# Kernel optimization log

Hardware: AMD Instinct MI355X
Metric: run time of the kernel (lower is better)

## Reference

```python
import jax, jax.numpy as jnp
import numpy as np

D_MODEL = 1024
NUM_HEADS = 16
HEAD_DIM = D_MODEL // NUM_HEADS


def setup_inputs() -> dict:
    key = jax.random.key(0)
    ks = jax.random.split(key, 9)
    s = 0.02
    return {
        "x": jax.random.normal(ks[0], (4, 2048, D_MODEL), dtype=jnp.float32),
        "Wq": jax.random.normal(ks[1], (D_MODEL, D_MODEL), dtype=jnp.float32) * s,
        "bq": jnp.zeros((D_MODEL,), dtype=jnp.float32),
        "Wk": jax.random.normal(ks[2], (D_MODEL, D_MODEL), dtype=jnp.float32) * s,
        "bk": jnp.zeros((D_MODEL,), dtype=jnp.float32),
        "Wv": jax.random.normal(ks[3], (D_MODEL, D_MODEL), dtype=jnp.float32) * s,
        "bv": jnp.zeros((D_MODEL,), dtype=jnp.float32),
        "Wo": jax.random.normal(ks[4], (D_MODEL, D_MODEL), dtype=jnp.float32) * s,
        "bo": jnp.zeros((D_MODEL,), dtype=jnp.float32),
    }


def reference(x, Wq, bq, Wk, bk, Wv, bv, Wo, bo):
    B, S, D = x.shape
    H, Hd = NUM_HEADS, HEAD_DIM

    def split_heads(t):  # [B,S,D] -> [B,H,S,Hd]
        return t.reshape(B, S, H, Hd).transpose(0, 2, 1, 3)

    q = split_heads(x @ Wq + bq)
    k = split_heads(x @ Wk + bk)
    v = split_heads(x @ Wv + bv)

    scale = 1.0 / jnp.sqrt(jnp.float32(Hd))
    scores = jnp.einsum("bhqd,bhkd->bhqk", q, k) * scale  # [B,H,S,S]
    attn = jax.nn.softmax(scores, axis=-1)
    # dropout(p=0.1) is identity in eval mode
    ctx = jnp.einsum("bhqk,bhkd->bhqd", attn, v)
    ctx = ctx.transpose(0, 2, 1, 3).reshape(B, S, D)
    return ctx @ Wo + bo
```

## Files before the change

kernel.cpp:

```cpp
#include <hip/hip_runtime.h>
#include <hip/hip_bf16.h>

typedef __bf16 bf16;
typedef bf16 bf16x8 __attribute__((ext_vector_type(8)));
typedef bf16 bf16x4v __attribute__((ext_vector_type(4)));
typedef bf16 bf16x2v __attribute__((ext_vector_type(2)));
typedef float f32x4 __attribute__((ext_vector_type(4)));
typedef float f32x16 __attribute__((ext_vector_type(16)));
typedef unsigned int uint;
typedef uint uint4v __attribute__((ext_vector_type(4)));

#define D_MODEL 1024
#define SEQ     2048
#define BATCH   4
#define NHEAD   16
#define HDIM    64
#define MTOK    8192
#define RSZ     ((size_t)MTOK * D_MODEL)
#define QSCALE  0.18033688011112042f

#define GLD16(src, dst)                                                        \
  __builtin_amdgcn_global_load_lds(                                            \
      (const __attribute__((address_space(1))) void*)(src),                    \
      (__attribute__((address_space(3))) void*)(dst), 16, 0, 0)

#define PSWAP(a, b) asm("v_permlane32_swap_b32 %0, %1" : "+v"(a), "+v"(b))

__device__ __forceinline__ uint pk2(float lo, float hi) {
  bf16x2v h;
  h[0] = (bf16)lo;
  h[1] = (bf16)hi;
  return __builtin_bit_cast(uint, h);
}

__global__ __launch_bounds__(256) void cvt_x_kernel(const float* __restrict__ x,
                                                    bf16* __restrict__ xb) {
  int i = blockIdx.x * 256 + threadIdx.x;
  f32x4 v = ((const f32x4*)x)[i];
  bf16x4v o;
#pragma unroll
  for (int c = 0; c < 4; ++c) o[c] = (bf16)v[c];
  ((bf16x4v*)xb)[i] = o;
}

__global__ __launch_bounds__(256) void wtrans_kernel(
    const float* __restrict__ Wq, const float* __restrict__ Wk,
    const float* __restrict__ Wv, const float* __restrict__ Wo,
    bf16* __restrict__ wt, bf16* __restrict__ wot) {
  __shared__ float t[32][33];
  int z = blockIdx.z;
  const float* W = (z == 0) ? Wq : (z == 1) ? Wk : (z == 2) ? Wv : Wo;
  bf16* dst = (z < 3) ? (wt + (size_t)z * D_MODEL * D_MODEL) : wot;
  int tx = threadIdx.x, ty = threadIdx.y;
  int bx = blockIdx.x * 32, by = blockIdx.y * 32;
#pragma unroll
  for (int j = 0; j < 4; ++j)
    t[ty + j * 8][tx] = W[(size_t)(by + ty + j * 8) * D_MODEL + bx + tx];
  __syncthreads();
#pragma unroll
  for (int j = 0; j < 4; ++j)
    dst[(size_t)(bx + ty + j * 8) * D_MODEL + by + tx] = (bf16)t[tx][ty + j * 8];
}

template <int MODE>
__global__ __launch_bounds__(256) void gemm_bt(
    const bf16* __restrict__ A, const bf16* __restrict__ Bt,
    const float* __restrict__ bias0, const float* __restrict__ bias1,
    const float* __restrict__ bias2, void* __restrict__ outp) {
  __shared__ bf16 As[128 * 32];
  __shared__ bf16 Bs[128 * 32];
  const int tid = threadIdx.x;
  const int wave = tid >> 6, lane = tid & 63;
  const int rowBase = blockIdx.y * 128;
  const int colBase = blockIdx.x * 128;
  const int wR = (wave >> 1) * 64;
  const int wC = (wave & 1) * 64;

  const int r0 = tid >> 2, c0 = tid & 3;
  const int cp0 = c0 ^ ((r0 >> 1) & 3);
  const int r1 = 64 + r0;
  const int cp1 = c0 ^ ((r1 >> 1) & 3);
  const bf16* srcA0 = A + (size_t)(rowBase + r0) * 1024 + cp0 * 8;
  const bf16* srcA1 = A + (size_t)(rowBase + r1) * 1024 + cp1 * 8;
  const bf16* srcB0 = Bt + (size_t)(colBase + r0) * 1024 + cp0 * 8;
  const bf16* srcB1 = Bt + (size_t)(colBase + r1) * 1024 + cp1 * 8;
  char* AsB = (char*)As;
  char* BsB = (char*)Bs;
  char* ldsA0 = AsB + wave * 1024;
  char* ldsA1 = AsB + 4096 + wave * 1024;
  char* ldsB0 = BsB + wave * 1024;
  char* ldsB1 = BsB + 4096 + wave * 1024;

  int aoff[4], boff[4];
#pragma unroll
  for (int i = 0; i < 4; ++i) {
    int ra = wR + i * 16 + (lane & 15);
    aoff[i] = ra * 64 + (((lane >> 4) ^ ((ra >> 1) & 3)) * 16);
    int rb = wC + i * 16 + (lane & 15);
    boff[i] = rb * 64 + (((lane >> 4) ^ ((rb >> 1) & 3)) * 16);
  }

  f32x4 acc[4][4] = {};
  for (int k0 = 0; k0 < 1024; k0 += 32) {
    GLD16(srcA0 + k0, ldsA0);
    GLD16(srcA1 + k0, ldsA1);
    GLD16(srcB0 + k0, ldsB0);
    GLD16(srcB1 + k0, ldsB1);
    __syncthreads();
    bf16x8 af[4], bf_[4];
#pragma unroll
    for (int i = 0; i < 4; ++i) af[i] = *(const bf16x8*)(AsB + aoff[i]);
#pragma unroll
    for (int i = 0; i < 4; ++i) bf_[i] = *(const bf16x8*)(BsB + boff[i]);
#pragma unroll
    for (int mi = 0; mi < 4; ++mi)
#pragma unroll
      for (int ni = 0; ni < 4; ++ni)
        acc[mi][ni] =
            __builtin_amdgcn_mfma_f32_16x16x32_bf16(af[mi], bf_[ni], acc[mi][ni], 0, 0, 0);
    __syncthreads();
  }

  const int rl = (lane >> 4) * 4;
  const int cl = lane & 15;
  if (MODE == 0) {
    bf16* qkvb = (bf16*)outp;
#pragma unroll
    for (int mi = 0; mi < 4; ++mi) {
      int rbase = rowBase + wR + mi * 16 + rl;
#pragma unroll
      for (int ni = 0; ni < 4; ++ni) {
        int col = colBase + wC + ni * 16 + cl;
        int mat = col >> 10, nn = col & 1023;
        int hh = nn >> 6, dd = nn & 63;
        if (mat == 2) {
          float bvv = bias2[nn];
          bf16x4v p4;
#pragma unroll
          for (int r = 0; r < 4; ++r) p4[r] = (bf16)(acc[mi][ni][r] + bvv);
          int bb = rbase >> 11, ss = rbase & 2047;
          *(bf16x4v*)(qkvb + 2 * RSZ +
                      ((size_t)(bb * NHEAD + hh) * HDIM + dd) * SEQ + ss) = p4;
        } else {
          const float* bp = (mat == 0) ? bias0 : bias1;
          float scl = (mat == 0) ? QSCALE : 1.0f;
          float bvv = bp[nn];
          bf16* dst = qkvb + (size_t)mat * RSZ;
#pragma unroll
          for (int r = 0; r < 4; ++r) {
            int m = rbase + r;
            int bb = m >> 11, ss = m & 2047;
            dst[((size_t)(bb * NHEAD + hh) * SEQ + ss) * HDIM + dd] =
                (bf16)((acc[mi][ni][r] + bvv) * scl);
          }
        }
      }
    }
  } else {
    float* dst = (float*)outp;
#pragma unroll
    for (int mi = 0; mi < 4; ++mi) {
      int rbase = rowBase + wR + mi * 16 + rl;
#pragma unroll
      for (int ni = 0; ni < 4; ++ni) {
        int col = colBase + wC + ni * 16 + cl;
        float bvv = bias0[col];
#pragma unroll
        for (int r = 0; r < 4; ++r)
          dst[(size_t)(rbase + r) * 1024 + col] = acc[mi][ni][r] + bvv;
      }
    }
  }
}

__global__ __launch_bounds__(256, 3) void attn_kernel(const bf16* __restrict__ qkv,
                                                      bf16* __restrict__ ctx) {
  __shared__ __align__(16) char smem[32768];
  char* Kbuf = smem;
  char* Vbuf = smem + 16384;

  const int tid = threadIdx.x;
  const int wave = tid >> 6, lane = tid & 63;
  const int l31 = lane & 31, l5 = lane >> 5;
  const int qt = blockIdx.x, hh = blockIdx.y, bb = blockIdx.z;
  const int bh = bb * NHEAD + hh;
  const bf16* Qp = qkv + (size_t)bh * SEQ * HDIM;
  const bf16* Kp = qkv + RSZ + (size_t)bh * SEQ * HDIM;
  const bf16* Vtp = qkv + 2 * RSZ + (size_t)bh * HDIM * SEQ;

  const int qrow = qt * 128 + wave * 32 + l31;
  bf16x8 qf[4];
#pragma unroll
  for (int kc = 0; kc < 4; ++kc)
    qf[kc] = *(const bf16x8*)(Qp + (size_t)qrow * 64 + kc * 16 + l5 * 8);

  const int sr = tid >> 3;
  const int sz = (tid & 7) ^ (sr & 7);
  const bf16* srcK0 = Kp + sr * 64 + sz * 8;
  const bf16* srcK1 = Kp + (sr + 32) * 64 + sz * 8;
  const bf16* srcV0 = Vtp + (size_t)sr * SEQ + sz * 8;
  const bf16* srcV1 = Vtp + (size_t)(sr + 32) * SEQ + sz * 8;

#define STAGE(sel, t)                                                     \
  do {                                                                    \
    GLD16(srcK0 + (t) * 4096, Kbuf + (sel) * 8192 + wave * 1024);         \
    GLD16(srcK1 + (t) * 4096, Kbuf + (sel) * 8192 + 4096 + wave * 1024);  \
    GLD16(srcV0 + (t) * 64, Vbuf + (sel) * 8192 + wave * 1024);           \
    GLD16(srcV1 + (t) * 64, Vbuf + (sel) * 8192 + 4096 + wave * 1024);    \
  } while (0)

  f32x16 o[2];
#pragma unroll
  for (int nd = 0; nd < 2; ++nd)
#pragma unroll
    for (int r = 0; r < 16; ++r) o[nd][r] = 0.f;
  float m_run = -1e30f, l_run = 0.f;

  STAGE(0, 0);
  __syncthreads();

  for (int kt = 0; kt < 32; ++kt) {
    const int cur = kt & 1;
    if (kt < 31) STAGE(cur ^ 1, kt + 1);

    const char* Kc = Kbuf + cur * 8192;
    const char* Vc = Vbuf + cur * 8192;

    f32x16 s[2];
#pragma unroll
    for (int nb = 0; nb < 2; ++nb)
#pragma unroll
      for (int r = 0; r < 16; ++r) s[nb][r] = 0.f;
#pragma unroll
    for (int nb = 0; nb < 2; ++nb)
#pragma unroll
      for (int kc = 0; kc < 4; ++kc) {
        int row = nb * 32 + l31;
        int off = row * 128 + (((2 * kc + l5) ^ (row & 7)) * 16);
        bf16x8 kf = *(const bf16x8*)(Kc + off);
        s[nb] = __builtin_amdgcn_mfma_f32_32x32x16_bf16(kf, qf[kc], s[nb], 0, 0, 0);
      }

    float t8[8];
#pragma unroll
    for (int r = 0; r < 8; ++r)
      t8[r] = fmaxf(fmaxf(s[0][r], s[0][r + 8]), fmaxf(s[1][r], s[1][r + 8]));
#pragma unroll
    for (int r = 0; r < 4; ++r) t8[r] = fmaxf(t8[r], t8[r + 4]);
    float pmax = fmaxf(fmaxf(t8[0], t8[1]), fmaxf(t8[2], t8[3]));
    pmax = fmaxf(pmax, __shfl_xor(pmax, 32, 64));

    if (!__all(pmax - m_run <= 8.0f)) {
      float mnew = fmaxf(m_run, pmax);
      float al = __builtin_amdgcn_exp2f(m_run - mnew);
      m_run = mnew;
      l_run *= al;
#pragma unroll
      for (int nd = 0; nd < 2; ++nd)
#pragma unroll
        for (int r = 0; r < 16; ++r) o[nd][r] *= al;
    }
#pragma unroll
    for (int nb = 0; nb < 2; ++nb)
#pragma unroll
      for (int r = 0; r < 16; ++r)
        s[nb][r] = __builtin_amdgcn_exp2f(s[nb][r] - m_run);

    f32x16 tv = s[0] + s[1];
    float q8[8];
#pragma unroll
    for (int r = 0; r < 8; ++r) q8[r] = tv[r] + tv[r + 8];
#pragma unroll
    for (int r = 0; r < 4; ++r) q8[r] += q8[r + 4];
    float rs = (q8[0] + q8[1]) + (q8[2] + q8[3]);
    rs += __shfl_xor(rs, 32, 64);
    l_run += rs;

    bf16x8 pf[4];
#pragma unroll
    for (int cc = 0; cc < 4; ++cc) {
      const int nb = cc >> 1, b0 = (cc & 1) * 8;
      uint w0 = pk2(s[nb][b0 + 0], s[nb][b0 + 1]);
      uint w1 = pk2(s[nb][b0 + 2], s[nb][b0 + 3]);
      uint w2 = pk2(s[nb][b0 + 4], s[nb][b0 + 5]);
      uint w3 = pk2(s[nb][b0 + 6], s[nb][b0 + 7]);
      PSWAP(w0, w2);
      PSWAP(w1, w3);
      uint4v u = {w0, w1, w2, w3};
      pf[cc] = __builtin_bit_cast(bf16x8, u);
    }

#pragma unroll
    for (int nd = 0; nd < 2; ++nd)
#pragma unroll
      for (int cc = 0; cc < 4; ++cc) {
        int row = nd * 32 + l31;
        int off = row * 128 + (((2 * cc + l5) ^ (row & 7)) * 16);
        bf16x8 vf = *(const bf16x8*)(Vc + off);
        o[nd] = __builtin_amdgcn_mfma_f32_32x32x16_bf16(vf, pf[cc], o[nd], 0, 0, 0);
      }
    __syncthreads();
  }

  const float inv = 1.0f / l_run;
  bf16* crow = ctx + (size_t)(bb * SEQ + qrow) * D_MODEL + hh * HDIM;
#pragma unroll
  for (int nd = 0; nd < 2; ++nd)
#pragma unroll
    for (int a = 0; a < 4; ++a) {
      bf16x4v p4;
#pragma unroll
      for (int b = 0; b < 4; ++b) p4[b] = (bf16)(o[nd][4 * a + b] * inv);
      *(bf16x4v*)(crow + nd * 32 + a * 8 + l5 * 4) = p4;
    }
#undef STAGE
}

extern "C" void kernel_launch(void* const* d_in, const int* in_sizes, int n_in,
                              void* d_out, int out_size, void* d_ws, size_t ws_size,
                              hipStream_t stream) {
  const float* x  = (const float*)d_in[0];
  const float* Wq = (const float*)d_in[1];
  const float* bq = (const float*)d_in[2];
  const float* Wk = (const float*)d_in[3];
  const float* bk = (const float*)d_in[4];
  const float* Wv = (const float*)d_in[5];
  const float* bv = (const float*)d_in[6];
  const float* Wo = (const float*)d_in[7];
  const float* bo = (const float*)d_in[8];

  char* ws = (char*)d_ws;
  bf16* xb   = (bf16*)(ws);
  bf16* wt   = (bf16*)(ws + (size_t)16 * 1024 * 1024);
  bf16* wot  = (bf16*)(ws + (size_t)22 * 1024 * 1024);
  bf16* qkvb = (bf16*)(ws + (size_t)24 * 1024 * 1024);
  bf16* ctxb = (bf16*)(ws + (size_t)72 * 1024 * 1024);

  cvt_x_kernel<<<8192, 256, 0, stream>>>(x, xb);
  wtrans_kernel<<<dim3(32, 32, 4), dim3(32, 8), 0, stream>>>(Wq, Wk, Wv, Wo, wt, wot);
  gemm_bt<0><<<dim3(24, 64), 256, 0, stream>>>(xb, wt, bq, bk, bv, (void*)qkvb);
  attn_kernel<<<dim3(16, 16, 4), 256, 0, stream>>>(qkvb, ctxb);
  gemm_bt<1><<<dim3(8, 64), 256, 0, stream>>>(ctxb, wot, bo, bo, bo, d_out);
}
```

Before: 295.8 us.

## Double-buffer GEMM LDS loads, swizzle block order for XCDs, add MFMA priority hints

The GEMM now double-buffers its A/B tiles in LDS, prefetching the next K slice while computing the current one. It replaces __syncthreads with explicit vmcnt waits plus raw barriers in both the GEMM and the attention kernel. Both kernels switch to 1D grids with a block-index swizzle that groups neighbouring tiles per XCD for better L2 locality, and the attention kernel raises wave priority around its MFMA sections. This doubles GEMM LDS use (lower occupancy risk) and depends on the hand-counted vmcnt values being correct.

```diff
diff --git a/kernel.cpp b/kernel.cpp
--- a/kernel.cpp
+++ b/kernel.cpp
@@ -23,6 +23,9 @@
   __builtin_amdgcn_global_load_lds(                                            \
       (const __attribute__((address_space(1))) void*)(src),                    \
       (__attribute__((address_space(3))) void*)(dst), 16, 0, 0)
+
+#define WAITVM(N) asm volatile("s_waitcnt vmcnt(" #N ")" ::: "memory")
+#define BAR() __builtin_amdgcn_s_barrier()
 
 #define PSWAP(a, b) asm("v_permlane32_swap_b32 %0, %1" : "+v"(a), "+v"(b))
 
@@ -67,12 +70,15 @@
     const bf16* __restrict__ A, const bf16* __restrict__ Bt,
     const float* __restrict__ bias0, const float* __restrict__ bias1,
     const float* __restrict__ bias2, void* __restrict__ outp) {
-  __shared__ bf16 As[128 * 32];
-  __shared__ bf16 Bs[128 * 32];
+  __shared__ bf16 As[2][128 * 32];
+  __shared__ bf16 Bs[2][128 * 32];
   const int tid = threadIdx.x;
   const int wave = tid >> 6, lane = tid & 63;
-  const int rowBase = blockIdx.y * 128;
-  const int colBase = blockIdx.x * 128;
+
+  const int nwg = gridDim.x;
+  const int swz = (blockIdx.x & 7) * (nwg >> 3) + (blockIdx.x >> 3);
+  const int rowBase = (swz & 63) * 128;
+  const int colBase = (swz >> 6) * 128;
   const int wR = (wave >> 1) * 64;
   const int wC = (wave & 1) * 64;
 
@@ -84,12 +90,14 @@
   const bf16* srcA1 = A + (size_t)(rowBase + r1) * 1024 + cp1 * 8;
   const bf16* srcB0 = Bt + (size_t)(colBase + r0) * 1024 + cp0 * 8;
   const bf16* srcB1 = Bt + (size_t)(colBase + r1) * 1024 + cp1 * 8;
-  char* AsB = (char*)As;
-  char* BsB = (char*)Bs;
-  char* ldsA0 = AsB + wave * 1024;
-  char* ldsA1 = AsB + 4096 + wave * 1024;
-  char* ldsB0 = BsB + wave * 1024;
-  char* ldsB1 = BsB + 4096 + wave * 1024;
+
+#define GSTAGE(sel, k0)                                                  \
+  do {                                                                   \
+    GLD16(srcA0 + (k0), (char*)As[sel] + wave * 1024);                   \
+    GLD16(srcA1 + (k0), (char*)As[sel] + 4096 + wave * 1024);            \
+    GLD16(srcB0 + (k0), (char*)Bs[sel] + wave * 1024);                   \
+    GLD16(srcB1 + (k0), (char*)Bs[sel] + 4096 + wave * 1024);            \
+  } while (0)
 
   int aoff[4], boff[4];
 #pragma unroll
@@ -101,12 +109,18 @@
   }
 
   f32x4 acc[4][4] = {};
-  for (int k0 = 0; k0 < 1024; k0 += 32) {
-    GLD16(srcA0 + k0, ldsA0);
-    GLD16(srcA1 + k0, ldsA1);
-    GLD16(srcB0 + k0, ldsB0);
-    GLD16(srcB1 + k0, ldsB1);
-    __syncthreads();
+  GSTAGE(0, 0);
+  for (int t = 0; t < 32; ++t) {
+    const int cur = t & 1;
+    if (t < 31) {
+      GSTAGE(cur ^ 1, (t + 1) * 32);
+      WAITVM(4);
+    } else {
+      WAITVM(0);
+    }
+    BAR();
+    const char* AsB = (const char*)As[cur];
+    const char* BsB = (const char*)Bs[cur];
     bf16x8 af[4], bf_[4];
 #pragma unroll
     for (int i = 0; i < 4; ++i) af[i] = *(const bf16x8*)(AsB + aoff[i]);
@@ -118,8 +132,9 @@
       for (int ni = 0; ni < 4; ++ni)
         acc[mi][ni] =
             __builtin_amdgcn_mfma_f32_16x16x32_bf16(af[mi], bf_[ni], acc[mi][ni], 0, 0, 0);
-    __syncthreads();
+    BAR();
   }
+#undef GSTAGE
 
   const int rl = (lane >> 4) * 4;
   const int cl = lane & 15;
@@ -182,7 +197,8 @@
   const int tid = threadIdx.x;
   const int wave = tid >> 6, lane = tid & 63;
   const int l31 = lane & 31, l5 = lane >> 5;
-  const int qt = blockIdx.x, hh = blockIdx.y, bb = blockIdx.z;
+  const int swz = (blockIdx.x & 7) * 128 + (blockIdx.x >> 3);
+  const int qt = swz & 15, hh = (swz >> 4) & 15, bb = swz >> 8;
   const int bh = bb * NHEAD + hh;
   const bf16* Qp = qkv + (size_t)bh * SEQ * HDIM;
   const bf16* Kp = qkv + RSZ + (size_t)bh * SEQ * HDIM;
@@ -217,11 +233,16 @@
   float m_run = -1e30f, l_run = 0.f;
 
   STAGE(0, 0);
-  __syncthreads();
 
   for (int kt = 0; kt < 32; ++kt) {
     const int cur = kt & 1;
-    if (kt < 31) STAGE(cur ^ 1, kt + 1);
+    if (kt < 31) {
+      STAGE(cur ^ 1, kt + 1);
+      WAITVM(4);
+    } else {
+      WAITVM(0);
+    }
+    BAR();
 
     const char* Kc = Kbuf + cur * 8192;
     const char* Vc = Vbuf + cur * 8192;
@@ -231,6 +252,7 @@
     for (int nb = 0; nb < 2; ++nb)
 #pragma unroll
       for (int r = 0; r < 16; ++r) s[nb][r] = 0.f;
+    __builtin_amdgcn_s_setprio(1);
 #pragma unroll
     for (int nb = 0; nb < 2; ++nb)
 #pragma unroll
@@ -240,6 +262,7 @@
         bf16x8 kf = *(const bf16x8*)(Kc + off);
         s[nb] = __builtin_amdgcn_mfma_f32_32x32x16_bf16(kf, qf[kc], s[nb], 0, 0, 0);
       }
+    __builtin_amdgcn_s_setprio(0);
 
     float t8[8];
 #pragma unroll
@@ -290,6 +313,7 @@
       pf[cc] = __builtin_bit_cast(bf16x8, u);
     }
 
+    __builtin_amdgcn_s_setprio(1);
 #pragma unroll
     for (int nd = 0; nd < 2; ++nd)
 #pragma unroll
@@ -299,7 +323,8 @@
         bf16x8 vf = *(const bf16x8*)(Vc + off);
         o[nd] = __builtin_amdgcn_mfma_f32_32x32x16_bf16(vf, pf[cc], o[nd], 0, 0, 0);
       }
-    __syncthreads();
+    __builtin_amdgcn_s_setprio(0);
+    BAR();
   }
 
   const float inv = 1.0f / l_run;
@@ -338,7 +363,7 @@
 
   cvt_x_kernel<<<8192, 256, 0, stream>>>(x, xb);
   wtrans_kernel<<<dim3(32, 32, 4), dim3(32, 8), 0, stream>>>(Wq, Wk, Wv, Wo, wt, wot);
-  gemm_bt<0><<<dim3(24, 64), 256, 0, stream>>>(xb, wt, bq, bk, bv, (void*)qkvb);
-  attn_kernel<<<dim3(16, 16, 4), 256, 0, stream>>>(qkvb, ctxb);
-  gemm_bt<1><<<dim3(8, 64), 256, 0, stream>>>(ctxb, wot, bo, bo, bo, d_out);
-}
+  gemm_bt<0><<<1536, 256, 0, stream>>>(xb, wt, bq, bk, bv, (void*)qkvb);
+  attn_kernel<<<1024, 256, 0, stream>>>(qkvb, ctxb);
+  gemm_bt<1><<<512, 256, 0, stream>>>(ctxb, wot, bo, bo, bo, d_out);
+}
```

Result: slower. 319.2 us (+7.9%).

## Move V transpose to separate kernel, swizzle attention grid, relax LDS barrier waits

Applied to the files above, without the earlier changes.

The QKV GEMM now writes V in the same row-major head layout as Q and K, and a new kernel transposes V into a separate buffer that reuses the x workspace. The attention kernel remaps its flat grid so consecutive blocks spread across heads and batches. It replaces the end-of-iteration syncthreads with explicit vmcnt waits plus a barrier so the prefetch of the next tile overlaps compute. It also raises wave priority around the MFMA sections. The goal is to drop the scattered transposed stores from the GEMM epilogue and hide load latency, at the cost of an extra kernel launch and another full pass over V.

```diff
diff --git a/kernel.cpp b/kernel.cpp
--- a/kernel.cpp
+++ b/kernel.cpp
@@ -23,6 +23,9 @@
   __builtin_amdgcn_global_load_lds(                                            \
       (const __attribute__((address_space(1))) void*)(src),                    \
       (__attribute__((address_space(3))) void*)(dst), 16, 0, 0)
+
+#define WAITVM(N) asm volatile("s_waitcnt vmcnt(" #N ")" ::: "memory")
+#define BAR() __builtin_amdgcn_s_barrier()
 
 #define PSWAP(a, b) asm("v_permlane32_swap_b32 %0, %1" : "+v"(a), "+v"(b))
 
@@ -60,6 +63,28 @@
 #pragma unroll
   for (int j = 0; j < 4; ++j)
     dst[(size_t)(bx + ty + j * 8) * D_MODEL + by + tx] = (bf16)t[tx][ty + j * 8];
+}
+
+__global__ __launch_bounds__(256) void vtrans_kernel(const bf16* __restrict__ V,
+                                                     bf16* __restrict__ Vt) {
+  __shared__ bf16 Ls[128][72];
+  const int st = blockIdx.x, bh = blockIdx.y;
+  const bf16* src = V + ((size_t)bh * SEQ + st * 128) * HDIM;
+  bf16* dst = Vt + (size_t)bh * HDIM * SEQ + st * 128;
+  const int t = threadIdx.x;
+  const int r = t >> 3, d0 = (t & 7) * 8;
+#pragma unroll
+  for (int j = 0; j < 4; ++j)
+    *(bf16x8*)&Ls[r + j * 32][d0] = *(const bf16x8*)(src + (size_t)(r + j * 32) * HDIM + d0);
+  __syncthreads();
+  const int d = t & 63, sc = (t >> 6) * 32;
+#pragma unroll
+  for (int c = 0; c < 4; ++c) {
+    bf16x8 v;
+#pragma unroll
+    for (int i = 0; i < 8; ++i) v[i] = Ls[sc + c * 8 + i][d];
+    *(bf16x8*)(dst + (size_t)d * SEQ + sc + c * 8) = v;
+  }
 }
 
 template <int MODE>
@@ -133,26 +158,16 @@
         int col = colBase + wC + ni * 16 + cl;
         int mat = col >> 10, nn = col & 1023;
         int hh = nn >> 6, dd = nn & 63;
-        if (mat == 2) {
-          float bvv = bias2[nn];
-          bf16x4v p4;
-#pragma unroll
-          for (int r = 0; r < 4; ++r) p4[r] = (bf16)(acc[mi][ni][r] + bvv);
-          int bb = rbase >> 11, ss = rbase & 2047;
-          *(bf16x4v*)(qkvb + 2 * RSZ +
-                      ((size_t)(bb * NHEAD + hh) * HDIM + dd) * SEQ + ss) = p4;
-        } else {
-          const float* bp = (mat == 0) ? bias0 : bias1;
-          float scl = (mat == 0) ? QSCALE : 1.0f;
-          float bvv = bp[nn];
-          bf16* dst = qkvb + (size_t)mat * RSZ;
-#pragma unroll
-          for (int r = 0; r < 4; ++r) {
-            int m = rbase + r;
-            int bb = m >> 11, ss = m & 2047;
-            dst[((size_t)(bb * NHEAD + hh) * SEQ + ss) * HDIM + dd] =
-                (bf16)((acc[mi][ni][r] + bvv) * scl);
-          }
+        const float* bp = (mat == 0) ? bias0 : (mat == 1) ? bias1 : bias2;
+        float scl = (mat == 0) ? QSCALE : 1.0f;
+        float bvv = bp[nn];
+        bf16* dst = qkvb + (size_t)mat * RSZ;
+#pragma unroll
+        for (int r = 0; r < 4; ++r) {
+          int m = rbase + r;
+          int bb = m >> 11, ss = m & 2047;
+          dst[((size_t)(bb * NHEAD + hh) * SEQ + ss) * HDIM + dd] =
+              (bf16)((acc[mi][ni][r] + bvv) * scl);
         }
       }
     }
@@ -174,6 +189,7 @@
 }
 
 __global__ __launch_bounds__(256, 3) void attn_kernel(const bf16* __restrict__ qkv,
+                                                      const bf16* __restrict__ vt,
                                                       bf16* __restrict__ ctx) {
   __shared__ __align__(16) char smem[32768];
   char* Kbuf = smem;
@@ -182,11 +198,12 @@
   const int tid = threadIdx.x;
   const int wave = tid >> 6, lane = tid & 63;
   const int l31 = lane & 31, l5 = lane >> 5;
-  const int qt = blockIdx.x, hh = blockIdx.y, bb = blockIdx.z;
+  const int swz = (blockIdx.x & 7) * 128 + (blockIdx.x >> 3);
+  const int qt = swz & 15, hh = (swz >> 4) & 15, bb = swz >> 8;
   const int bh = bb * NHEAD + hh;
   const bf16* Qp = qkv + (size_t)bh * SEQ * HDIM;
   const bf16* Kp = qkv + RSZ + (size_t)bh * SEQ * HDIM;
-  const bf16* Vtp = qkv + 2 * RSZ + (size_t)bh * HDIM * SEQ;
+  const bf16* Vtp = vt + (size_t)bh * HDIM * SEQ;
 
   const int qrow = qt * 128 + wave * 32 + l31;
   bf16x8 qf[4];
@@ -217,11 +234,16 @@
   float m_run = -1e30f, l_run = 0.f;
 
   STAGE(0, 0);
-  __syncthreads();
 
   for (int kt = 0; kt < 32; ++kt) {
     const int cur = kt & 1;
-    if (kt < 31) STAGE(cur ^ 1, kt + 1);
+    if (kt < 31) {
+      STAGE(cur ^ 1, kt + 1);
+      WAITVM(4);
+    } else {
+      WAITVM(0);
+    }
+    BAR();
 
     const char* Kc = Kbuf + cur * 8192;
     const char* Vc = Vbuf + cur * 8192;
@@ -231,6 +253,7 @@
     for (int nb = 0; nb < 2; ++nb)
 #pragma unroll
       for (int r = 0; r < 16; ++r) s[nb][r] = 0.f;
+    __builtin_amdgcn_s_setprio(1);
 #pragma unroll
     for (int nb = 0; nb < 2; ++nb)
 #pragma unroll
@@ -240,6 +263,7 @@
         bf16x8 kf = *(const bf16x8*)(Kc + off);
         s[nb] = __builtin_amdgcn_mfma_f32_32x32x16_bf16(kf, qf[kc], s[nb], 0, 0, 0);
       }
+    __builtin_amdgcn_s_setprio(0);
 
     float t8[8];
 #pragma unroll
@@ -290,6 +314,7 @@
       pf[cc] = __builtin_bit_cast(bf16x8, u);
     }
 
+    __builtin_amdgcn_s_setprio(1);
 #pragma unroll
     for (int nd = 0; nd < 2; ++nd)
 #pragma unroll
@@ -299,7 +324,8 @@
         bf16x8 vf = *(const bf16x8*)(Vc + off);
         o[nd] = __builtin_amdgcn_mfma_f32_32x32x16_bf16(vf, pf[cc], o[nd], 0, 0, 0);
       }
-    __syncthreads();
+    __builtin_amdgcn_s_setprio(0);
+    BAR();
   }
 
   const float inv = 1.0f / l_run;
@@ -331,6 +357,7 @@
 
   char* ws = (char*)d_ws;
   bf16* xb   = (bf16*)(ws);
+  bf16* vtb  = (bf16*)(ws);
   bf16* wt   = (bf16*)(ws + (size_t)16 * 1024 * 1024);
   bf16* wot  = (bf16*)(ws + (size_t)22 * 1024 * 1024);
   bf16* qkvb = (bf16*)(ws + (size_t)24 * 1024 * 1024);
@@ -339,6 +366,7 @@
   cvt_x_kernel<<<8192, 256, 0, stream>>>(x, xb);
   wtrans_kernel<<<dim3(32, 32, 4), dim3(32, 8), 0, stream>>>(Wq, Wk, Wv, Wo, wt, wot);
   gemm_bt<0><<<dim3(24, 64), 256, 0, stream>>>(xb, wt, bq, bk, bv, (void*)qkvb);
-  attn_kernel<<<dim3(16, 16, 4), 256, 0, stream>>>(qkvb, ctxb);
+  vtrans_kernel<<<dim3(16, 64), 256, 0, stream>>>(qkvb + 2 * RSZ, vtb);
+  attn_kernel<<<1024, 256, 0, stream>>>(qkvb, vtb, ctxb);
   gemm_bt<1><<<dim3(8, 64), 256, 0, stream>>>(ctxb, wot, bo, bo, bo, d_out);
 }
```

Result: slower. 303.8 us (+2.7%).
